# Optimization experiments

Hardware: AMD Instinct MI355X
Metric: run time of the kernel (lower is better)

## Reference

```python
import jax, jax.numpy as jnp
import numpy as np

B, S, H = 2, 2048, 4096
NQ, NKV, D = 32, 8, 128  # query heads, kv heads, head_dim
G = NQ // NKV            # GQA group size
NEG = -1e9


def _rope_tables(seq_len, dim, base=10000.0):
    inv = 1.0 / (base ** (jnp.arange(0, dim, 2, dtype=jnp.float32) / dim))
    t = jnp.arange(seq_len, dtype=jnp.float32)
    freqs = jnp.outer(t, inv)                      # [S, D/2]
    emb = jnp.concatenate([freqs, freqs], axis=-1)  # [S, D]
    return jnp.cos(emb), jnp.sin(emb)


def _rotate_half(x):
    d = x.shape[-1] // 2
    return jnp.concatenate([-x[..., d:], x[..., :d]], axis=-1)


def setup_inputs() -> dict:
    key = jax.random.key(0)
    k1, k2, k3, k4, k5 = jax.random.split(key, 5)
    hidden_states = jax.random.normal(k1, (B, S, 2 * H), dtype=jnp.float32)
    # additive causal mask [1,1,S,S]
    causal = jnp.tril(jnp.ones((S, S), dtype=bool))
    attention_mask = jnp.where(causal, 0.0, NEG).astype(jnp.float32)[None, None]
    cos, sin = _rope_tables(S, D)
    sc = 1.0 / np.sqrt(2 * H)
    Wq = jax.random.normal(k2, (NQ * D, 2 * H), dtype=jnp.float32) * sc
    Wk = jax.random.normal(k3, (NKV * D, 2 * H), dtype=jnp.float32) * sc
    Wv = jax.random.normal(k4, (NKV * D, 2 * H), dtype=jnp.float32) * sc
    Wo = jax.random.normal(k5, (H, NQ * D), dtype=jnp.float32) * (1.0 / np.sqrt(NQ * D))
    return dict(hidden_states=hidden_states, attention_mask=attention_mask,
                cos=cos, sin=sin, Wq=Wq, Wk=Wk, Wv=Wv, Wo=Wo)


def reference(hidden_states, attention_mask, cos, sin, Wq, Wk, Wv, Wo):
    bsz, q_len, _ = hidden_states.shape
    # projections: [B,S,heads*D] -> [B,heads,S,D]
    q = (hidden_states @ Wq.T).reshape(bsz, q_len, NQ, D).transpose(0, 2, 1, 3)
    k = (hidden_states @ Wk.T).reshape(bsz, q_len, NKV, D).transpose(0, 2, 1, 3)
    v = (hidden_states @ Wv.T).reshape(bsz, q_len, NKV, D).transpose(0, 2, 1, 3)
    # RoPE (cos/sin broadcast over batch, heads)
    c = cos[None, None]  # [1,1,S,D]
    s = sin[None, None]
    q = q * c + _rotate_half(q) * s
    k = k * c + _rotate_half(k) * s
    # GQA: group query heads [B, NKV, G, S, D] against shared K/V (same math as repeat_kv)
    qg = q.reshape(bsz, NKV, G, q_len, D)
    scores = jnp.einsum('bkgsd,bktd->bkgst', qg, k) / np.sqrt(D)
    scores = scores + attention_mask  # [1,1,S,S] broadcasts over (G,S,T)
    probs = jax.nn.softmax(scores.astype(jnp.float32), axis=-1).astype(q.dtype)
    out = jnp.einsum('bkgst,bktd->bkgsd', probs, v)
    out = out.reshape(bsz, NQ, q_len, D).transpose(0, 2, 1, 3).reshape(bsz, q_len, NQ * D)
    return out @ Wo.T
```

## Files before the change

kernel.cpp:

```cpp
#include <hip/hip_runtime.h>
#include <stdint.h>

typedef __attribute__((ext_vector_type(8))) short bf8;
typedef __attribute__((ext_vector_type(4))) float f4;

__device__ __forceinline__ float bf2f(uint16_t u) {
  union { unsigned i; float f; } v; v.i = ((unsigned)u) << 16; return v.f;
}
__device__ __forceinline__ uint16_t f2bf(float f) {
  union { float f; unsigned i; } v; v.f = f;
  unsigned r = v.i + 0x7fffu + ((v.i >> 16) & 1u);
  return (uint16_t)(r >> 16);
}
__device__ __forceinline__ bf8 cvt8(float4 a, float4 b) {
  bf8 r;
  r[0]=(short)f2bf(a.x); r[1]=(short)f2bf(a.y); r[2]=(short)f2bf(a.z); r[3]=(short)f2bf(a.w);
  r[4]=(short)f2bf(b.x); r[5]=(short)f2bf(b.y); r[6]=(short)f2bf(b.z); r[7]=(short)f2bf(b.w);
  return r;
}
__device__ __forceinline__ uint32_t cvtpk(float a, float b) {
  uint32_t r;
  asm("v_cvt_pk_bf16_f32 %0, %1, %2" : "=v"(r) : "v"(a), "v"(b));
  return r;
}

__device__ __forceinline__ void gload_lds16(const void* g, void* l) {
  __builtin_amdgcn_global_load_lds(
      (const __attribute__((address_space(1))) uint32_t*)(uintptr_t)g,
      (__attribute__((address_space(3))) uint32_t*)(uint32_t)(uintptr_t)l,
      16, 0, 0);
}

__global__ __launch_bounds__(256)
void eagle3_cvt(const float* __restrict__ src, uint16_t* __restrict__ dst, int n8)
{
  int i = blockIdx.x * 256 + threadIdx.x;
  const int stride = gridDim.x * 256;
  for (; i < n8; i += stride) {
    const float4 a = ((const float4*)src)[i * 2];
    const float4 b = ((const float4*)src)[i * 2 + 1];
    ((bf8*)dst)[i] = cvt8(a, b);
  }
}

template<bool OF32>
__global__ __launch_bounds__(256)
void eagle3_gemm2(const uint16_t* __restrict__ Ap, const uint16_t* __restrict__ Bp,
                  void* __restrict__ Cp, int K, int lda, int ldb, int ldc)
{
  __shared__ __align__(16) uint16_t As[128 * 32];
  __shared__ __align__(16) uint16_t Bs[128 * 32];

  const int nwg = gridDim.x * gridDim.y;
  const int bid = blockIdx.y * gridDim.x + blockIdx.x;
  const int qq = nwg >> 3;
  const int sw = (bid & 7) * qq + (bid >> 3);
  const int bx = sw % gridDim.x, by = sw / gridDim.x;
  const int m0 = by * 128, n0 = bx * 128;

  const int tid = threadIdx.x, lane = tid & 63, w = tid >> 6;
  const int tl = lane & 15, g = lane >> 4;
  const int wr = (w >> 1) * 64, wc = (w & 1) * 64;

  f4 acc[4][4] = {};

  for (int k0 = 0; k0 < K; k0 += 32) {
    __syncthreads();
    #pragma unroll
    for (int i = 0; i < 2; ++i) {
      const int o = (w * 2 + i) * 1024 + lane * 16;
      const int r = o >> 6;
      const int u = (((o >> 4) & 3) ^ ((r >> 1) & 3)) * 8;
      gload_lds16(Ap + (size_t)(m0 + r) * lda + k0 + u, &As[(w * 2 + i) * 512]);
    }
    #pragma unroll
    for (int i = 0; i < 2; ++i) {
      const int o = (w * 2 + i) * 1024 + lane * 16;
      const int r = o >> 6;
      const int u = (((o >> 4) & 3) ^ ((r >> 1) & 3)) * 8;
      gload_lds16(Bp + (size_t)(n0 + r) * ldb + k0 + u, &Bs[(w * 2 + i) * 512]);
    }
    __syncthreads();

    bf8 af[4], bf_[4];
    #pragma unroll
    for (int i = 0; i < 4; ++i) {
      const int ar = wr + i * 16 + tl;
      const int br = wc + i * 16 + tl;
      af[i]  = *(const bf8*)&As[ar * 32 + ((g ^ ((ar >> 1) & 3)) * 8)];
      bf_[i] = *(const bf8*)&Bs[br * 32 + ((g ^ ((br >> 1) & 3)) * 8)];
    }
    #pragma unroll
    for (int mi = 0; mi < 4; ++mi)
      #pragma unroll
      for (int ni = 0; ni < 4; ++ni)
        acc[mi][ni] = __builtin_amdgcn_mfma_f32_16x16x32_bf16(af[mi], bf_[ni], acc[mi][ni], 0, 0, 0);
  }

  #pragma unroll
  for (int mi = 0; mi < 4; ++mi) {
    #pragma unroll
    for (int r = 0; r < 4; ++r) {
      const int row = m0 + wr + mi * 16 + g * 4 + r;
      #pragma unroll
      for (int ni = 0; ni < 4; ++ni) {
        const int col = n0 + wc + ni * 16 + tl;
        const float v = acc[mi][ni][r];
        if constexpr (OF32) ((float*)Cp)[(size_t)row * ldc + col] = v;
        else                ((uint16_t*)Cp)[(size_t)row * ldc + col] = f2bf(v);
      }
    }
  }
}

template<bool OF32>
__global__ __launch_bounds__(512, 2)
void eagle3_gemm5(const uint16_t* __restrict__ Ap, const uint16_t* __restrict__ Bp,
                  void* __restrict__ Cp, int K, int lda, int ldb, int ldc)
{
  __shared__ __align__(16) uint16_t As[2][2][128 * 64];
  __shared__ __align__(16) uint16_t Bs[2][2][128 * 64];

  int bx, by;
  const int bid = blockIdx.y * gridDim.x + blockIdx.x;
  if (gridDim.x == 16 && gridDim.y == 16) {
    const int x = bid & 7, j = bid >> 3;
    by = (x >> 1) * 4 + (j >> 3);
    bx = (x & 1) * 8 + (j & 7);
  } else {
    const int nwg = gridDim.x * gridDim.y;
    const int qq = nwg >> 3;
    const int sw = (bid & 7) * qq + (bid >> 3);
    bx = sw % gridDim.x; by = sw / gridDim.x;
  }
  const int m0 = by * 256, n0 = bx * 256;

  const int tid = threadIdx.x, lane = tid & 63;
  const int tl = lane & 15, g = lane >> 4;
  const int w = tid >> 6;
  const int wm = w >> 2, wn = w & 3;
  const int bhf = wn >> 1;
  const int bl0 = (wn & 1) * 64;

  f4 acc[8][4] = {};
  const int NI = K >> 7;

  const int jr = tid >> 3;
  const int jc = ((tid & 7) ^ (jr & 7)) * 8;
  #define STG_A(slot, h, tt)                                                    \
    { const int kk_ = (tt) << 6;                                                \
      gload_lds16(Ap + (size_t)(m0 + (h)*128 + jr) * lda + kk_ + jc,            \
                  &As[slot][h][tid * 8]);                                       \
      gload_lds16(Ap + (size_t)(m0 + (h)*128 + 64 + jr) * lda + kk_ + jc,       \
                  &As[slot][h][(tid + 512) * 8]); }
  #define STG_B(slot, h, tt)                                                    \
    { const int kk_ = (tt) << 6;                                                \
      gload_lds16(Bp + (size_t)(n0 + (h)*128 + jr) * ldb + kk_ + jc,            \
                  &Bs[slot][h][tid * 8]);                                       \
      gload_lds16(Bp + (size_t)(n0 + (h)*128 + 64 + jr) * ldb + kk_ + jc,       \
                  &Bs[slot][h][(tid + 512) * 8]); }

  const int rk0 = ((0 + g) ^ (tl & 7)) * 8;
  const int rk1 = ((4 + g) ^ (tl & 7)) * 8;

  bf8 af[8], b0[4], b1[4];
  #define READ_A(slot, rh)                                                      \
    { _Pragma("unroll")                                                         \
      for (int m_ = 0; m_ < 4; ++m_) {                                          \
        const int R_ = (rh)*64 + m_*16 + tl;                                    \
        af[m_*2]   = *(const bf8*)&As[slot][wm][R_*64 + rk0];                   \
        af[m_*2+1] = *(const bf8*)&As[slot][wm][R_*64 + rk1];                   \
      } }
  #define READ_B(slot, ch, dst)                                                 \
    { _Pragma("unroll")                                                         \
      for (int c_ = 0; c_ < 2; ++c_) {                                          \
        const int R_ = bl0 + (ch)*32 + c_*16 + tl;                              \
        dst[c_*2]   = *(const bf8*)&Bs[slot][bhf][R_*64 + rk0];                 \
        dst[c_*2+1] = *(const bf8*)&Bs[slot][bhf][R_*64 + rk1];                 \
      } }
  #define MID_SYNC                                                              \
    __builtin_amdgcn_sched_barrier(0);                                          \
    __builtin_amdgcn_s_barrier();                                               \
    asm volatile("s_waitcnt lgkmcnt(0)" ::: "memory");                          \
    __builtin_amdgcn_sched_barrier(0);
  #define CLOSE_BAR                                                             \
    __builtin_amdgcn_sched_barrier(0);                                          \
    __builtin_amdgcn_s_barrier();                                               \
    __builtin_amdgcn_sched_barrier(0);
  #define MFMA16(rh, ch, bsrc)                                                  \
    { __builtin_amdgcn_s_setprio(1);                                            \
      _Pragma("unroll")                                                         \
      for (int m_ = 0; m_ < 4; ++m_) {                                          \
        _Pragma("unroll")                                                       \
        for (int c_ = 0; c_ < 2; ++c_) {                                        \
          acc[(rh)*4+m_][(ch)*2+c_] = __builtin_amdgcn_mfma_f32_16x16x32_bf16(  \
              af[m_*2],   bsrc[c_*2],   acc[(rh)*4+m_][(ch)*2+c_], 0, 0, 0);    \
          acc[(rh)*4+m_][(ch)*2+c_] = __builtin_amdgcn_mfma_f32_16x16x32_bf16(  \
              af[m_*2+1], bsrc[c_*2+1], acc[(rh)*4+m_][(ch)*2+c_], 0, 0, 0);    \
        } }                                                                     \
      __builtin_amdgcn_s_setprio(0); }

  STG_A(0, 0, 0); STG_A(0, 1, 0); STG_B(0, 0, 0); STG_B(0, 1, 0);
  STG_B(1, 0, 1); STG_B(1, 1, 1);
  asm volatile("s_waitcnt vmcnt(4)" ::: "memory");
  CLOSE_BAR;
  READ_B(0, 0, b0);

  for (int i = 0; i < NI; ++i) {
    const int T1 = 2 * i + 1;
    const bool more = (i + 1 < NI);

    READ_A(0, 0);
    STG_A(1, 0, T1);
    MID_SYNC; MFMA16(0, 0, b0); CLOSE_BAR;

    READ_B(0, 1, b1);
    STG_A(1, 1, T1);
    MID_SYNC; MFMA16(0, 1, b1); CLOSE_BAR;

    READ_A(0, 1);
    if (more) STG_B(0, 0, T1 + 1);
    MID_SYNC; MFMA16(1, 0, b0);
    if (more) { asm volatile("s_waitcnt vmcnt(6)" ::: "memory"); }
    else      { asm volatile("s_waitcnt vmcnt(4)" ::: "memory"); }
    CLOSE_BAR;

    READ_B(1, 0, b0);
    if (more) STG_B(0, 1, T1 + 1);
    MID_SYNC; MFMA16(1, 1, b1);
    if (more) { asm volatile("s_waitcnt vmcnt(4)" ::: "memory"); }
    else      { asm volatile("s_waitcnt vmcnt(0)" ::: "memory"); }
    CLOSE_BAR;

    READ_A(1, 0);
    if (more) STG_A(0, 0, T1 + 1);
    MID_SYNC; MFMA16(0, 0, b0); CLOSE_BAR;

    READ_B(1, 1, b1);
    if (more) STG_A(0, 1, T1 + 1);
    MID_SYNC; MFMA16(0, 1, b1); CLOSE_BAR;

    READ_A(1, 1);
    if (more) STG_B(1, 0, T1 + 2);
    MID_SYNC; MFMA16(1, 0, b0);
    if (more) { asm volatile("s_waitcnt vmcnt(6)" ::: "memory"); }
    CLOSE_BAR;

    if (more) { READ_B(0, 0, b0); STG_B(1, 1, T1 + 2); }
    MID_SYNC; MFMA16(1, 1, b1);
    if (more) { asm volatile("s_waitcnt vmcnt(4)" ::: "memory"); }
    CLOSE_BAR;
  }
  #undef STG_A
  #undef STG_B
  #undef READ_A
  #undef READ_B
  #undef MID_SYNC
  #undef CLOSE_BAR
  #undef MFMA16

  const int wr = wm * 128, wc = wn * 64;
  #pragma unroll
  for (int mi = 0; mi < 8; ++mi) {
    #pragma unroll
    for (int r = 0; r < 4; ++r) {
      const int row = m0 + wr + mi * 16 + g * 4 + r;
      #pragma unroll
      for (int ni = 0; ni < 4; ++ni) {
        const int col = n0 + wc + ni * 16 + tl;
        const float v = acc[mi][ni][r];
        if constexpr (OF32) ((float*)Cp)[(size_t)row * ldc + col] = v;
        else                ((uint16_t*)Cp)[(size_t)row * ldc + col] = f2bf(v);
      }
    }
  }
}

__global__ __launch_bounds__(256)
void eagle3_rope(uint16_t* __restrict__ x, const float* __restrict__ cs,
                 const float* __restrict__ sn, int nh, int rowlen, int total)
{
  int id = blockIdx.x * 256 + threadIdx.x;
  if (id >= total) return;
  int d = id & 63;
  int t = id >> 6;
  int head = t & (nh - 1);
  int row = t / nh;
  int s = row & 2047;
  size_t base = (size_t)row * rowlen + head * 128;
  float c = cs[s * 128 + d], si = sn[s * 128 + d];
  float x1 = bf2f(x[base + d]), x2 = bf2f(x[base + d + 64]);
  x[base + d]      = f2bf(x1 * c - x2 * si);
  x[base + d + 64] = f2bf(x2 * c + x1 * si);
}

__global__ __launch_bounds__(256)
void eagle3_vtrans(const uint16_t* __restrict__ V, uint16_t* __restrict__ Vt)
{
  __shared__ uint16_t T[64 * 136];
  const int tid = threadIdx.x;
  const int t0 = blockIdx.x * 64;
  const int bh = blockIdx.y;
  const int b = bh >> 3, h = bh & 7;
  {
    const int r = tid >> 2, c0 = (tid & 3) * 32;
    const uint16_t* src = V + (size_t)(b * 2048 + t0 + r) * 1024 + h * 128 + c0;
    #pragma unroll
    for (int j = 0; j < 4; ++j)
      *(bf8*)&T[r * 136 + c0 + j * 8] = *(const bf8*)(src + j * 8);
  }
  __syncthreads();
  {
    const int d = tid >> 1, tc = (tid & 1) * 32;
    uint16_t* dst = Vt + ((size_t)bh * 128 + d) * 2048 + t0 + tc;
    #pragma unroll
    for (int cc = 0; cc < 4; ++cc) {
      bf8 v;
      #pragma unroll
      for (int j = 0; j < 8; ++j) v[j] = T[(tc + cc * 8 + j) * 136 + d];
      *(bf8*)&dst[cc * 8] = v;
    }
  }
}

__global__ __launch_bounds__(512, 4)
void eagle3_flash7(const uint16_t* __restrict__ Q, const uint16_t* __restrict__ Kt,
                   const uint16_t* __restrict__ Vt, uint16_t* __restrict__ O,
                   const float* __restrict__ Cst, const float* __restrict__ Snt)
{
  __shared__ __align__(16) uint16_t Ks[2][64 * 128];
  __shared__ __align__(16) uint16_t Vs[2][128 * 64];
  __shared__ __align__(16) uint16_t Pl[8][16 * 64];

  const int tid = threadIdx.x, lane = tid & 63, w = tid >> 6;
  const int tl = lane & 15, g = lane >> 4;

  const int bid = (int)blockIdx.x + ((int)blockIdx.y << 4) + ((int)blockIdx.z << 9);
  const int xcd = bid & 7, idx = bid >> 3;
  const int grp = xcd * 2 + (idx >> 6);
  const int j   = idx & 63;
  const int b = grp >> 3, hkv = grp & 7;
  const int hq = hkv * 4 + (j & 3);
  const int qt = 15 - (j >> 2);
  const int qrow0 = qt * 128 + w * 16;
  const int ntb = 2 * qt + 2;

  bf8 qf[4];
  {
    const int srow = qrow0 + tl;
    const uint16_t* qp = Q + ((size_t)(b * 2048 + srow)) * 4096 + hq * 128 + g * 8;
    #pragma unroll
    for (int kb = 0; kb < 4; ++kb) qf[kb] = *(const bf8*)(qp + kb * 32);
    const float* cp = Cst + (size_t)srow * 128 + g * 8;
    const float* sp = Snt + (size_t)srow * 128 + g * 8;
    #pragma unroll
    for (int kb = 0; kb < 2; ++kb) {
      const float4 c0 = *(const float4*)(cp + kb * 32);
      const float4 c1 = *(const float4*)(cp + kb * 32 + 4);
      const float4 s0 = *(const float4*)(sp + kb * 32);
      const float4 s1 = *(const float4*)(sp + kb * 32 + 4);
      const float cc[8] = {c0.x,c0.y,c0.z,c0.w,c1.x,c1.y,c1.z,c1.w};
      const float ss[8] = {s0.x,s0.y,s0.z,s0.w,s1.x,s1.y,s1.z,s1.w};
      #pragma unroll
      for (int e = 0; e < 8; ++e) {
        const float x1 = bf2f((uint16_t)qf[kb][e]);
        const float x2 = bf2f((uint16_t)qf[kb + 2][e]);
        qf[kb][e]     = (short)f2bf(x1 * cc[e] - x2 * ss[e]);
        qf[kb + 2][e] = (short)f2bf(x2 * cc[e] + x1 * ss[e]);
      }
    }
  }

  const uint16_t* Kbase = Kt + (size_t)b * 2048 * 1024 + hkv * 128;
  const uint16_t* Vtb   = Vt + ((size_t)(b * 8 + hkv) * 128) * 2048;

  bf8 onesf = {};
  if (tl == 0) {
    #pragma unroll
    for (int q8 = 0; q8 < 8; ++q8) onesf[q8] = (short)0x3F80;
  }

  f4 acc[8] = {};
  f4 accl = {};
  float rm[4] = {-3e38f, -3e38f, -3e38f, -3e38f};
  const float KS = 0.1275174f;

  #define STAGE_TILE(buf, t0s)                                                   \
    {                                                                            \
      _Pragma("unroll")                                                          \
      for (int i = 0; i < 2; ++i) {                                              \
        const int f = i * 512 + tid;                                             \
        const int r = f >> 4, c = f & 15;                                        \
        gload_lds16(Kbase + (size_t)((t0s) + r) * 1024 + ((c ^ (r & 7)) * 8),    \
                    &Ks[buf][(i * 512 + w * 64) * 8]);                           \
      }                                                                          \
      _Pragma("unroll")                                                          \
      for (int i = 0; i < 2; ++i) {                                              \
        const int f = i * 512 + tid;                                             \
        const int d = f >> 3, c = f & 7;                                         \
        gload_lds16(Vtb + (size_t)d * 2048 + (t0s) + ((c ^ (d & 7)) * 8),        \
                    &Vs[buf][(i * 512 + w * 64) * 8]);                           \
      }                                                                          \
    }

  STAGE_TILE(0, 0);

  for (int tb = 0; tb < ntb; ++tb) {
    const int cur = tb & 1;
    const int t0 = tb * 64;

    if (tb + 1 < ntb) {
      STAGE_TILE(cur ^ 1, t0 + 64);
      asm volatile("s_waitcnt vmcnt(4)" ::: "memory");
    } else {
      asm volatile("s_waitcnt vmcnt(0)" ::: "memory");
    }
    __builtin_amdgcn_sched_barrier(0);
    __builtin_amdgcn_s_barrier();

    const bool active = (t0 <= qrow0 + 15);
    if (active) {
      f4 s[4] = {};
      __builtin_amdgcn_s_setprio(1);
      #pragma unroll
      for (int cf = 0; cf < 4; ++cf) {
        #pragma unroll
        for (int kb = 0; kb < 4; ++kb) {
          const bf8 kf = *(const bf8*)&Ks[cur][(cf * 16 + tl) * 128 +
                                              (((kb * 4 + g) ^ (tl & 7)) * 8)];
          s[cf] = __builtin_amdgcn_mfma_f32_16x16x32_bf16(qf[kb], kf, s[cf], 0, 0, 0);
        }
      }
      __builtin_amdgcn_s_setprio(0);

      const bool edge = (t0 + 63 > qrow0);
      float p[4][4];
      #pragma unroll
      for (int r = 0; r < 4; ++r) {
        float v[4];
        #pragma unroll
        for (int cf = 0; cf < 4; ++cf) v[cf] = s[cf][r];
        if (edge) {
          const int qg = qrow0 + g * 4 + r;
          #pragma unroll
          for (int cf = 0; cf < 4; ++cf)
            if (t0 + cf * 16 + tl > qg) v[cf] = -3e38f;
        }
        float mx = fmaxf(fmaxf(v[0], v[1]), fmaxf(v[2], v[3]));
        mx = fmaxf(mx, __shfl_xor(mx, 1));
        mx = fmaxf(mx, __shfl_xor(mx, 2));
        mx = fmaxf(mx, __shfl_xor(mx, 4));
        mx = fmaxf(mx, __shfl_xor(mx, 8));
        if (mx > rm[r]) {
          const float corr = exp2f((rm[r] - mx) * KS);
          #pragma unroll
          for (int df = 0; df < 8; ++df) acc[df][r] *= corr;
          accl[r] *= corr;
          rm[r] = mx;
        }
        #pragma unroll
        for (int cf = 0; cf < 4; ++cf) p[r][cf] = exp2f((v[cf] - rm[r]) * KS);
      }

      #pragma unroll
      for (int r = 0; r < 4; ++r) {
        const uint32_t pk0 = cvtpk(p[r][0], p[r][1]);
        const uint32_t pk1 = cvtpk(p[r][2], p[r][3]);
        const int row = g * 4 + r;
        const int sw = row & 7;
        uint16_t* Pw = &Pl[w][row * 64 + (tl & 7)];
        Pw[(((tl >> 3) + 0) ^ sw) * 8] = (uint16_t)pk0;
        Pw[(((tl >> 3) + 2) ^ sw) * 8] = (uint16_t)(pk0 >> 16);
        Pw[(((tl >> 3) + 4) ^ sw) * 8] = (uint16_t)pk1;
        Pw[(((tl >> 3) + 6) ^ sw) * 8] = (uint16_t)(pk1 >> 16);
      }
      const bf8 pf0 = *(const bf8*)&Pl[w][tl * 64 + ((g ^ (tl & 7)) * 8)];
      const bf8 pf1 = *(const bf8*)&Pl[w][tl * 64 + (((4 + g) ^ (tl & 7)) * 8)];

      __builtin_amdgcn_s_setprio(1);
      accl = __builtin_amdgcn_mfma_f32_16x16x32_bf16(pf0, onesf, accl, 0, 0, 0);
      accl = __builtin_amdgcn_mfma_f32_16x16x32_bf16(pf1, onesf, accl, 0, 0, 0);
      #pragma unroll
      for (int df = 0; df < 8; ++df) {
        const int vrow = (df * 16 + tl) * 64;
        const bf8 v0 = *(const bf8*)&Vs[cur][vrow + ((g ^ (tl & 7)) * 8)];
        const bf8 v1 = *(const bf8*)&Vs[cur][vrow + (((4 + g) ^ (tl & 7)) * 8)];
        acc[df] = __builtin_amdgcn_mfma_f32_16x16x32_bf16(pf0, v0, acc[df], 0, 0, 0);
        acc[df] = __builtin_amdgcn_mfma_f32_16x16x32_bf16(pf1, v1, acc[df], 0, 0, 0);
      }
      __builtin_amdgcn_s_setprio(0);
    }

    __builtin_amdgcn_s_barrier();
  }
  #undef STAGE_TILE

  #pragma unroll
  for (int r = 0; r < 4; ++r) {
    const float l = __shfl(accl[r], lane & 48);
    const float inv = 1.0f / l;
    const size_t ob = ((size_t)(b * 2048 + qrow0 + g * 4 + r)) * 4096 + hq * 128 + tl;
    #pragma unroll
    for (int df = 0; df < 8; ++df)
      O[ob + df * 16] = f2bf(acc[df][r] * inv);
  }
}

extern "C" void kernel_launch(void* const* d_in, const int* in_sizes, int n_in,
                              void* d_out, int out_size, void* d_ws, size_t ws_size,
                              hipStream_t stream) {
  const float* hs   = (const float*)d_in[0];
  const float* cosT = (const float*)d_in[2];
  const float* sinT = (const float*)d_in[3];
  const float* Wq   = (const float*)d_in[4];
  const float* Wk   = (const float*)d_in[5];
  const float* Wv   = (const float*)d_in[6];
  const float* Wo   = (const float*)d_in[7];

  char* ws = (char*)d_ws;
  uint16_t* qb    = (uint16_t*)(ws);
  uint16_t* kbuf  = (uint16_t*)(ws + 33554432);
  uint16_t* vbuf  = (uint16_t*)(ws + 41943040);
  uint16_t* whalf = (uint16_t*)(ws + 50331648);
  uint16_t* vt    = (uint16_t*)(ws + 75497472);
  uint16_t* ctx   = (uint16_t*)(ws + 41943040);
  uint16_t* hsb   = (uint16_t*)d_out;
  uint16_t* wobf  = qb;

  const dim3 blk(256);
  const bool fullq = (ws_size >= (size_t)117440512);

  eagle3_cvt<<<dim3(2048), blk, 0, stream>>>(hs, hsb, 4194304);

  if (fullq) {
    eagle3_cvt<<<dim3(2048), blk, 0, stream>>>(Wq, whalf, 4194304);
    eagle3_gemm5<false><<<dim3(16, 16), dim3(512), 0, stream>>>(
        hsb, whalf, (void*)qb, 8192, 8192, 8192, 4096);
  } else {
    eagle3_cvt<<<dim3(2048), blk, 0, stream>>>(Wq, whalf, 2097152);
    eagle3_gemm2<false><<<dim3(16, 32), blk, 0, stream>>>(
        hsb, whalf, (void*)qb, 8192, 8192, 8192, 4096);
    eagle3_cvt<<<dim3(2048), blk, 0, stream>>>(Wq + 16777216, whalf, 2097152);
    eagle3_gemm2<false><<<dim3(16, 32), blk, 0, stream>>>(
        hsb, whalf, (void*)(qb + 2048), 8192, 8192, 8192, 4096);
  }

  eagle3_cvt<<<dim3(2048), blk, 0, stream>>>(Wk, whalf, 1048576);
  eagle3_gemm2<false><<<dim3(8, 32), blk, 0, stream>>>(
      hsb, whalf, (void*)kbuf, 8192, 8192, 8192, 1024);
  eagle3_cvt<<<dim3(2048), blk, 0, stream>>>(Wv, whalf, 1048576);
  eagle3_gemm2<false><<<dim3(8, 32), blk, 0, stream>>>(
      hsb, whalf, (void*)vbuf, 8192, 8192, 8192, 1024);

  eagle3_rope<<<dim3(8192), blk, 0, stream>>>(kbuf, cosT, sinT, 8, 1024, 2097152);
  eagle3_vtrans<<<dim3(32, 16), blk, 0, stream>>>(vbuf, vt);

  eagle3_flash7<<<dim3(16, 32, 2), dim3(512), 0, stream>>>(
      qb, kbuf, vt, ctx, cosT, sinT);

  eagle3_cvt<<<dim3(2048), blk, 0, stream>>>(Wo, wobf, 2097152);
  eagle3_gemm5<true><<<dim3(16, 16), dim3(512), 0, stream>>>(
      ctx, wobf, d_out, 4096, 4096, 4096, 4096);
}
```

Before: 904.2 us.

## Fuse K/V projections into one GEMM with in-epilogue RoPE and batched weight casts

Merges the separate K and V projection GEMMs into a single launch over a concatenated K|V weight, applying RoPE to K in the epilogue through an LDS staging tile. This removes the standalone rope kernel and its read-modify-write pass over K. It also merges the Wk, Wv and Wo fp32-to-bf16 casts into one launch and drops the fallback path for a smaller workspace, so the code now assumes the larger workspace. Costs are extra LDS per block (which may reduce occupancy) and divergent epilogue branches.

```diff
diff --git a/kernel.cpp b/kernel.cpp
--- a/kernel.cpp
+++ b/kernel.cpp
@@ -43,13 +43,34 @@
   }
 }
 
-template<bool OF32>
 __global__ __launch_bounds__(256)
-void eagle3_gemm2(const uint16_t* __restrict__ Ap, const uint16_t* __restrict__ Bp,
-                  void* __restrict__ Cp, int K, int lda, int ldb, int ldc)
+void eagle3_cvt3(const float* __restrict__ s1, uint16_t* __restrict__ d1, int n1,
+                 const float* __restrict__ s2, uint16_t* __restrict__ d2, int n2,
+                 const float* __restrict__ s3, uint16_t* __restrict__ d3, int n3)
+{
+  int i = blockIdx.x * 256 + threadIdx.x;
+  const int stride = gridDim.x * 256;
+  const int tot = n1 + n2 + n3;
+  for (; i < tot; i += stride) {
+    const float* src; uint16_t* dst; int j;
+    if (i < n1)           { src = s1; dst = d1; j = i; }
+    else if (i < n1 + n2) { src = s2; dst = d2; j = i - n1; }
+    else                  { src = s3; dst = d3; j = i - n1 - n2; }
+    const float4 a = ((const float4*)src)[j * 2];
+    const float4 b = ((const float4*)src)[j * 2 + 1];
+    ((bf8*)dst)[j] = cvt8(a, b);
+  }
+}
+
+__global__ __launch_bounds__(256)
+void eagle3_gemmkv(const uint16_t* __restrict__ Ap, const uint16_t* __restrict__ Bp,
+                   uint16_t* __restrict__ Kc, uint16_t* __restrict__ Vc,
+                   const float* __restrict__ Cst, const float* __restrict__ Snt)
 {
   __shared__ __align__(16) uint16_t As[128 * 32];
   __shared__ __align__(16) uint16_t Bs[128 * 32];
+  __shared__ __align__(16) uint16_t Kx[128 * 130];
+  const int K = 8192, lda = 8192, ldb = 8192;
 
   const int nwg = gridDim.x * gridDim.y;
   const int bid = blockIdx.y * gridDim.x + blockIdx.x;
@@ -97,19 +118,48 @@
         acc[mi][ni] = __builtin_amdgcn_mfma_f32_16x16x32_bf16(af[mi], bf_[ni], acc[mi][ni], 0, 0, 0);
   }
 
-  #pragma unroll
-  for (int mi = 0; mi < 4; ++mi) {
-    #pragma unroll
-    for (int r = 0; r < 4; ++r) {
-      const int row = m0 + wr + mi * 16 + g * 4 + r;
-      #pragma unroll
-      for (int ni = 0; ni < 4; ++ni) {
-        const int col = n0 + wc + ni * 16 + tl;
-        const float v = acc[mi][ni][r];
-        if constexpr (OF32) ((float*)Cp)[(size_t)row * ldc + col] = v;
-        else                ((uint16_t*)Cp)[(size_t)row * ldc + col] = f2bf(v);
-      }
-    }
+  const bool isK = (n0 < 1024);
+  const int c0 = n0 & 1023;
+  if (isK) {
+    #pragma unroll
+    for (int mi = 0; mi < 4; ++mi)
+      #pragma unroll
+      for (int r = 0; r < 4; ++r) {
+        const int row = wr + mi * 16 + g * 4 + r;
+        #pragma unroll
+        for (int ni = 0; ni < 4; ++ni)
+          Kx[row * 130 + wc + ni * 16 + tl] = f2bf(acc[mi][ni][r]);
+      }
+    __syncthreads();
+    #pragma unroll
+    for (int mi = 0; mi < 4; ++mi)
+      #pragma unroll
+      for (int r = 0; r < 4; ++r) {
+        const int row = wr + mi * 16 + g * 4 + r;
+        const int s = (m0 + row) & 2047;
+        #pragma unroll
+        for (int ni = 0; ni < 4; ++ni) {
+          const int d = wc + ni * 16 + tl;
+          const float own = bf2f(Kx[row * 130 + d]);
+          const float oth = bf2f(Kx[row * 130 + (d ^ 64)]);
+          const float cv = Cst[s * 128 + d];
+          const float sv = Snt[s * 128 + d];
+          const float out = wc ? (own * cv + oth * sv) : (own * cv - oth * sv);
+          Kc[(size_t)(m0 + row) * 1024 + c0 + d] = f2bf(out);
+        }
+      }
+  } else {
+    #pragma unroll
+    for (int mi = 0; mi < 4; ++mi)
+      #pragma unroll
+      for (int r = 0; r < 4; ++r) {
+        const int row = m0 + wr + mi * 16 + g * 4 + r;
+        #pragma unroll
+        for (int ni = 0; ni < 4; ++ni) {
+          const int col = c0 + wc + ni * 16 + tl;
+          Vc[(size_t)row * 1024 + col] = f2bf(acc[mi][ni][r]);
+        }
+      }
   }
 }
 
@@ -277,24 +327,6 @@
 }
 
 __global__ __launch_bounds__(256)
-void eagle3_rope(uint16_t* __restrict__ x, const float* __restrict__ cs,
-                 const float* __restrict__ sn, int nh, int rowlen, int total)
-{
-  int id = blockIdx.x * 256 + threadIdx.x;
-  if (id >= total) return;
-  int d = id & 63;
-  int t = id >> 6;
-  int head = t & (nh - 1);
-  int row = t / nh;
-  int s = row & 2047;
-  size_t base = (size_t)row * rowlen + head * 128;
-  float c = cs[s * 128 + d], si = sn[s * 128 + d];
-  float x1 = bf2f(x[base + d]), x2 = bf2f(x[base + d + 64]);
-  x[base + d]      = f2bf(x1 * c - x2 * si);
-  x[base + d + 64] = f2bf(x2 * c + x1 * si);
-}
-
-__global__ __launch_bounds__(256)
 void eagle3_vtrans(const uint16_t* __restrict__ V, uint16_t* __restrict__ Vt)
 {
   __shared__ uint16_t T[64 * 136];
@@ -518,47 +550,34 @@
   const float* Wo   = (const float*)d_in[7];
 
   char* ws = (char*)d_ws;
-  uint16_t* qb    = (uint16_t*)(ws);
-  uint16_t* kbuf  = (uint16_t*)(ws + 33554432);
-  uint16_t* vbuf  = (uint16_t*)(ws + 41943040);
-  uint16_t* whalf = (uint16_t*)(ws + 50331648);
-  uint16_t* vt    = (uint16_t*)(ws + 75497472);
-  uint16_t* ctx   = (uint16_t*)(ws + 41943040);
-  uint16_t* hsb   = (uint16_t*)d_out;
-  uint16_t* wobf  = qb;
+  uint16_t* qb   = (uint16_t*)(ws);
+  uint16_t* kbuf = (uint16_t*)(ws + 33554432);
+  uint16_t* vbuf = (uint16_t*)(ws + 41943040);
+  uint16_t* wkv  = (uint16_t*)(ws + 50331648);
+  uint16_t* vt   = (uint16_t*)(ws + 75497472);
+  uint16_t* ctx  = (uint16_t*)(ws + 41943040);
+  uint16_t* wobf = (uint16_t*)(ws + 83886080);
+  uint16_t* hsb  = (uint16_t*)d_out;
 
   const dim3 blk(256);
-  const bool fullq = (ws_size >= (size_t)117440512);
 
   eagle3_cvt<<<dim3(2048), blk, 0, stream>>>(hs, hsb, 4194304);
 
-  if (fullq) {
-    eagle3_cvt<<<dim3(2048), blk, 0, stream>>>(Wq, whalf, 4194304);
-    eagle3_gemm5<false><<<dim3(16, 16), dim3(512), 0, stream>>>(
-        hsb, whalf, (void*)qb, 8192, 8192, 8192, 4096);
-  } else {
-    eagle3_cvt<<<dim3(2048), blk, 0, stream>>>(Wq, whalf, 2097152);
-    eagle3_gemm2<false><<<dim3(16, 32), blk, 0, stream>>>(
-        hsb, whalf, (void*)qb, 8192, 8192, 8192, 4096);
-    eagle3_cvt<<<dim3(2048), blk, 0, stream>>>(Wq + 16777216, whalf, 2097152);
-    eagle3_gemm2<false><<<dim3(16, 32), blk, 0, stream>>>(
-        hsb, whalf, (void*)(qb + 2048), 8192, 8192, 8192, 4096);
-  }
-
-  eagle3_cvt<<<dim3(2048), blk, 0, stream>>>(Wk, whalf, 1048576);
-  eagle3_gemm2<false><<<dim3(8, 32), blk, 0, stream>>>(
-      hsb, whalf, (void*)kbuf, 8192, 8192, 8192, 1024);
-  eagle3_cvt<<<dim3(2048), blk, 0, stream>>>(Wv, whalf, 1048576);
-  eagle3_gemm2<false><<<dim3(8, 32), blk, 0, stream>>>(
-      hsb, whalf, (void*)vbuf, 8192, 8192, 8192, 1024);
-
-  eagle3_rope<<<dim3(8192), blk, 0, stream>>>(kbuf, cosT, sinT, 8, 1024, 2097152);
+  eagle3_cvt<<<dim3(2048), blk, 0, stream>>>(Wq, wkv, 4194304);
+  eagle3_gemm5<false><<<dim3(16, 16), dim3(512), 0, stream>>>(
+      hsb, wkv, (void*)qb, 8192, 8192, 8192, 4096);
+
+  eagle3_cvt3<<<dim3(2048), blk, 0, stream>>>(
+      Wk, wkv, 1048576, Wv, wkv + 8388608, 1048576, Wo, wobf, 2097152);
+
+  eagle3_gemmkv<<<dim3(16, 32), blk, 0, stream>>>(
+      hsb, wkv, kbuf, vbuf, cosT, sinT);
+
   eagle3_vtrans<<<dim3(32, 16), blk, 0, stream>>>(vbuf, vt);
 
   eagle3_flash7<<<dim3(16, 32, 2), dim3(512), 0, stream>>>(
       qb, kbuf, vt, ctx, cosT, sinT);
 
-  eagle3_cvt<<<dim3(2048), blk, 0, stream>>>(Wo, wobf, 2097152);
   eagle3_gemm5<true><<<dim3(16, 16), dim3(512), 0, stream>>>(
       ctx, wobf, d_out, 4096, 4096, 4096, 4096);
 }
```

Result: faster. 750.2 us (-17.0%).
